# Kernel optimization log

Hardware: AMD Instinct MI355X
Metric: run time of the kernel (lower is better)

The kernel has to match this reference:

```python
import jax, jax.numpy as jnp
import numpy as np

R = 16
ALPHA = 32
SCALING = ALPHA / R  # 2.0


def setup_inputs() -> dict:
    key = jax.random.key(0)
    k_x, k_w, k_b, k_a, k_lb, k_o = jax.random.split(key, 6)
    in_f, out_f = 4096, 4096
    x = jax.random.normal(k_x, (4, 4096, in_f), dtype=jnp.float32)
    base_kernel = jax.random.normal(k_w, (in_f, out_f), dtype=jnp.float32) * 0.02
    base_bias = jax.random.normal(k_b, (out_f,), dtype=jnp.float32) * 0.02
    lora_A = jax.random.normal(k_a, (R, R), dtype=jnp.float32)
    lora_B = jax.random.normal(k_lb, (R, R), dtype=jnp.float32) * 0.02
    O = jax.random.normal(k_o, (in_f // R, out_f // R), dtype=jnp.float32)
    return {"x": x, "base_kernel": base_kernel, "base_bias": base_bias,
            "lora_A": lora_A, "lora_B": lora_B, "O": O}


def reference(x, base_kernel, base_bias, lora_A, lora_B, O) -> jnp.ndarray:
    in_f, out_f = base_kernel.shape
    # base path: x @ W + b
    base_out = jnp.dot(x, base_kernel) + base_bias
    # LoKr path: kron(A @ B, O) materialized as in the original module
    w_left = jnp.dot(lora_A, lora_B)                 # (r, r)
    lokr_update = jnp.kron(w_left, O)                # (r*in_factor, r*out_factor)
    lokr_update = lokr_update[:in_f, :out_f]
    lokr_out = jnp.dot(x, lokr_update)
    return base_out + lokr_out * SCALING
```

## Files before the change

kernel.cpp:

```cpp
#include <hip/hip_runtime.h>
#include <stdint.h>
#include <stddef.h>


#define M_TOT 16384
#define K_TOT 4096
#define N_TOT 4096
#define SCALING 2.0f

typedef __attribute__((ext_vector_type(8))) short bf16x8;
typedef __attribute__((ext_vector_type(4))) float floatx4;

__device__ __forceinline__ unsigned short f32_to_bf16(float f) {
  union { float f; unsigned int u; } v; v.f = f;
  unsigned int r = 0x7fffu + ((v.u >> 16) & 1u);
  return (unsigned short)((v.u + r) >> 16);
}

__device__ __forceinline__ void async_copy16(const void* gsrc, void* ldst) {
  __builtin_amdgcn_global_load_lds(
      (const __attribute__((address_space(1))) void*)(uintptr_t)gsrc,
      (__attribute__((address_space(3))) void*)(uintptr_t)ldst,
      16, 0, 0);
}

__global__ void wleft_kernel(const float* __restrict__ A, const float* __restrict__ B,
                             float* __restrict__ wl) {
  int i = threadIdx.x >> 4, j = threadIdx.x & 15;
  float s = 0.f;
#pragma unroll
  for (int k = 0; k < 16; ++k) s += A[i * 16 + k] * B[k * 16 + j];
  wl[threadIdx.x] = s * SCALING;
}

__global__ void prep_w_kernel(const float* __restrict__ base, const float* __restrict__ O,
                              const float* __restrict__ wl, unsigned short* __restrict__ Wt) {
  __shared__ float tile[32][33];
  int n0 = blockIdx.x * 32, k0 = blockIdx.y * 32;
  int tx = threadIdx.x, ty = threadIdx.y;
#pragma unroll
  for (int r = 0; r < 32; r += 8) {
    int k = k0 + ty + r, n = n0 + tx;
    float v = base[(size_t)k * N_TOT + n]
            + wl[((k >> 8) << 4) + (n >> 8)] * O[((size_t)(k & 255) << 8) + (n & 255)];
    tile[ty + r][tx] = v;
  }
  __syncthreads();
#pragma unroll
  for (int r = 0; r < 32; r += 8) {
    int n = n0 + ty + r, k = k0 + tx;
    Wt[(size_t)n * K_TOT + k] = f32_to_bf16(tile[tx][ty + r]);
  }
}

__global__ void cvt_x_kernel(const float* __restrict__ x, unsigned short* __restrict__ xb) {
  size_t i = ((size_t)blockIdx.x * blockDim.x + threadIdx.x) * 8;
  float4 a = *(const float4*)(x + i);
  float4 b = *(const float4*)(x + i + 4);
  union { bf16x8 v; unsigned short h[8]; } u;
  u.h[0] = f32_to_bf16(a.x); u.h[1] = f32_to_bf16(a.y);
  u.h[2] = f32_to_bf16(a.z); u.h[3] = f32_to_bf16(a.w);
  u.h[4] = f32_to_bf16(b.x); u.h[5] = f32_to_bf16(b.y);
  u.h[6] = f32_to_bf16(b.z); u.h[7] = f32_to_bf16(b.w);
  *(bf16x8*)(xb + i) = u.v;
}

__global__ __launch_bounds__(256) void gemm_bt_kernel(
    const unsigned short* __restrict__ Xb, const unsigned short* __restrict__ Wt,
    const float* __restrict__ bias, float* __restrict__ out) {
  __shared__ __align__(16) unsigned short Alds[128 * 32];
  __shared__ __align__(16) unsigned short Blds[128 * 32];

  const int tid = threadIdx.x;
  const int wave = tid >> 6, lane = tid & 63;
  const int quad = lane >> 4, lanemod = lane & 15;
  const int wm = wave & 1, wn = wave >> 1;

  const int m0 = blockIdx.y * 128, n0 = blockIdx.x * 128;

  floatx4 acc[4][4];
#pragma unroll
  for (int i = 0; i < 4; ++i)
#pragma unroll
    for (int j = 0; j < 4; ++j) acc[i][j] = (floatx4){0.f, 0.f, 0.f, 0.f};

  for (int k0 = 0; k0 < K_TOT; k0 += 32) {
#pragma unroll
    for (int it = 0; it < 2; ++it) {
      int c = it * 256 + tid;
      int row = c >> 2, kc = c & 3;
      async_copy16(Xb + ((size_t)(m0 + row) * K_TOT + k0 + kc * 8), Alds + (size_t)c * 8);
      async_copy16(Wt + ((size_t)(n0 + row) * K_TOT + k0 + kc * 8), Blds + (size_t)c * 8);
    }
    __syncthreads();

    bf16x8 af[4], bfr[4];
#pragma unroll
    for (int t = 0; t < 4; ++t) {
      af[t]  = *(const bf16x8*)(Alds + ((wm * 64 + t * 16 + lanemod) * 32 + quad * 8));
      bfr[t] = *(const bf16x8*)(Blds + ((wn * 64 + t * 16 + lanemod) * 32 + quad * 8));
    }
#pragma unroll
    for (int mt = 0; mt < 4; ++mt)
#pragma unroll
      for (int nt = 0; nt < 4; ++nt)
        acc[mt][nt] = __builtin_amdgcn_mfma_f32_16x16x32_bf16(af[mt], bfr[nt], acc[mt][nt], 0, 0, 0);
    __syncthreads();
  }

#pragma unroll
  for (int nt = 0; nt < 4; ++nt) {
    int col = n0 + wn * 64 + nt * 16 + lanemod;
    float bv = bias[col];
#pragma unroll
    for (int mt = 0; mt < 4; ++mt) {
      int row = m0 + wm * 64 + mt * 16 + quad * 4;
#pragma unroll
      for (int r = 0; r < 4; ++r)
        out[(size_t)(row + r) * N_TOT + col] = acc[mt][nt][r] + bv;
    }
  }
}

extern "C" void kernel_launch(void* const* d_in, const int* in_sizes, int n_in,
                              void* d_out, int out_size, void* d_ws, size_t ws_size,
                              hipStream_t stream) {
  const float* x    = (const float*)d_in[0];
  const float* base = (const float*)d_in[1];
  const float* bias = (const float*)d_in[2];
  const float* lA   = (const float*)d_in[3];
  const float* lB   = (const float*)d_in[4];
  const float* O    = (const float*)d_in[5];
  float* out = (float*)d_out;

  char* ws = (char*)d_ws;
  unsigned short* Xb = (unsigned short*)ws;
  unsigned short* Wt = (unsigned short*)(ws + (size_t)M_TOT * K_TOT * 2);
  float* wl = (float*)(ws + (size_t)M_TOT * K_TOT * 2 + (size_t)N_TOT * K_TOT * 2);

  wleft_kernel<<<1, 256, 0, stream>>>(lA, lB, wl);
  prep_w_kernel<<<dim3(N_TOT / 32, K_TOT / 32), dim3(32, 8), 0, stream>>>(base, O, wl, Wt);
  cvt_x_kernel<<<((size_t)M_TOT * K_TOT) / 8 / 256, 256, 0, stream>>>(x, Xb);
  gemm_bt_kernel<<<dim3(N_TOT / 128, M_TOT / 128), 256, 0, stream>>>(Xb, Wt, bias, out);
}
```

Baseline: 1.121 ms.

## Switch GEMM to 32x32x16 MFMA with swizzled LDS and grouped tile order

The GEMM kernel now uses 32x32x16 bf16 MFMA instructions on 2x2 accumulator tiles instead of 16x16x32 on 4x4 tiles. It XOR-swizzles the LDS layout to avoid bank conflicts on fragment reads, and it precomputes global source pointers that advance by 32 elements per step. Blocks launch on a 1D grid that is remapped so groups of 8 M-tiles share each N tile, which is meant to improve L2 reuse. The aim is to cut LDS read traffic and bank conflicts and raise MFMA throughput. It adds more complex index math and a different output write pattern.

```diff
diff --git a/kernel.cpp b/kernel.cpp
--- a/kernel.cpp
+++ b/kernel.cpp
@@ -9,6 +9,7 @@
 #define SCALING 2.0f
 
 typedef __attribute__((ext_vector_type(8))) short bf16x8;
+typedef __attribute__((ext_vector_type(16))) float floatx16;
 typedef __attribute__((ext_vector_type(4))) float floatx4;
 
 __device__ __forceinline__ unsigned short f32_to_bf16(float f) {
@@ -72,52 +73,75 @@
   __shared__ __align__(16) unsigned short Blds[128 * 32];
 
   const int tid = threadIdx.x;
-  const int wave = tid >> 6, lane = tid & 63;
-  const int quad = lane >> 4, lanemod = lane & 15;
+  const int lane = tid & 63;
+  const int wave = tid >> 6;
+  const int lane31 = lane & 31, khalf = lane >> 5;
   const int wm = wave & 1, wn = wave >> 1;
 
-  const int m0 = blockIdx.y * 128, n0 = blockIdx.x * 128;
+  const int bid = blockIdx.x;
+  const int grp = bid >> 8, loc = bid & 255;
+  const int m0 = (grp * 8 + (loc & 7)) * 128;
+  const int n0 = (loc >> 3) * 128;
 
-  floatx4 acc[4][4];
+  floatx16 acc[2][2];
 #pragma unroll
-  for (int i = 0; i < 4; ++i)
+  for (int i = 0; i < 2; ++i)
 #pragma unroll
-    for (int j = 0; j < 4; ++j) acc[i][j] = (floatx4){0.f, 0.f, 0.f, 0.f};
+    for (int j = 0; j < 2; ++j)
+#pragma unroll
+      for (int r = 0; r < 16; ++r) acc[i][j][r] = 0.f;
+
+  int c0 = tid, c1 = 256 + tid;
+  int r0 = c0 >> 2, s0 = c0 & 3, kc0 = s0 ^ ((r0 >> 1) & 3);
+  int r1 = c1 >> 2, s1 = c1 & 3, kc1 = s1 ^ ((r1 >> 1) & 3);
+  const unsigned short* srcA0 = Xb + (size_t)(m0 + r0) * K_TOT + kc0 * 8;
+  const unsigned short* srcA1 = Xb + (size_t)(m0 + r1) * K_TOT + kc1 * 8;
+  const unsigned short* srcB0 = Wt + (size_t)(n0 + r0) * K_TOT + kc0 * 8;
+  const unsigned short* srcB1 = Wt + (size_t)(n0 + r1) * K_TOT + kc1 * 8;
+
+  int arow0 = wm * 64 + 0 * 32 + lane31, arow1 = wm * 64 + 1 * 32 + lane31;
+  int brow0 = wn * 64 + 0 * 32 + lane31, brow1 = wn * 64 + 1 * 32 + lane31;
+  int aswz0 = (arow0 >> 1) & 3, aswz1 = (arow1 >> 1) & 3;
+  int bswz0 = (brow0 >> 1) & 3, bswz1 = (brow1 >> 1) & 3;
 
   for (int k0 = 0; k0 < K_TOT; k0 += 32) {
-#pragma unroll
-    for (int it = 0; it < 2; ++it) {
-      int c = it * 256 + tid;
-      int row = c >> 2, kc = c & 3;
-      async_copy16(Xb + ((size_t)(m0 + row) * K_TOT + k0 + kc * 8), Alds + (size_t)c * 8);
-      async_copy16(Wt + ((size_t)(n0 + row) * K_TOT + k0 + kc * 8), Blds + (size_t)c * 8);
-    }
+    async_copy16(srcA0, Alds + (size_t)c0 * 8);
+    async_copy16(srcA1, Alds + (size_t)c1 * 8);
+    async_copy16(srcB0, Blds + (size_t)c0 * 8);
+    async_copy16(srcB1, Blds + (size_t)c1 * 8);
+    srcA0 += 32; srcA1 += 32; srcB0 += 32; srcB1 += 32;
     __syncthreads();
 
-    bf16x8 af[4], bfr[4];
 #pragma unroll
-    for (int t = 0; t < 4; ++t) {
-      af[t]  = *(const bf16x8*)(Alds + ((wm * 64 + t * 16 + lanemod) * 32 + quad * 8));
-      bfr[t] = *(const bf16x8*)(Blds + ((wn * 64 + t * 16 + lanemod) * 32 + quad * 8));
+    for (int t = 0; t < 2; ++t) {
+      int jj = 2 * t + khalf;
+      bf16x8 a0 = *(const bf16x8*)(Alds + arow0 * 32 + (jj ^ aswz0) * 8);
+      bf16x8 a1 = *(const bf16x8*)(Alds + arow1 * 32 + (jj ^ aswz1) * 8);
+      bf16x8 b0 = *(const bf16x8*)(Blds + brow0 * 32 + (jj ^ bswz0) * 8);
+      bf16x8 b1 = *(const bf16x8*)(Blds + brow1 * 32 + (jj ^ bswz1) * 8);
+      acc[0][0] = __builtin_amdgcn_mfma_f32_32x32x16_bf16(a0, b0, acc[0][0], 0, 0, 0);
+      acc[0][1] = __builtin_amdgcn_mfma_f32_32x32x16_bf16(a0, b1, acc[0][1], 0, 0, 0);
+      acc[1][0] = __builtin_amdgcn_mfma_f32_32x32x16_bf16(a1, b0, acc[1][0], 0, 0, 0);
+      acc[1][1] = __builtin_amdgcn_mfma_f32_32x32x16_bf16(a1, b1, acc[1][1], 0, 0, 0);
     }
-#pragma unroll
-    for (int mt = 0; mt < 4; ++mt)
-#pragma unroll
-      for (int nt = 0; nt < 4; ++nt)
-        acc[mt][nt] = __builtin_amdgcn_mfma_f32_16x16x32_bf16(af[mt], bfr[nt], acc[mt][nt], 0, 0, 0);
     __syncthreads();
   }
 
 #pragma unroll
-  for (int nt = 0; nt < 4; ++nt) {
-    int col = n0 + wn * 64 + nt * 16 + lanemod;
+  for (int nt = 0; nt < 2; ++nt) {
+    int col = n0 + wn * 64 + nt * 32 + lane31;
     float bv = bias[col];
 #pragma unroll
-    for (int mt = 0; mt < 4; ++mt) {
-      int row = m0 + wm * 64 + mt * 16 + quad * 4;
+    for (int mt = 0; mt < 2; ++mt) {
+      int rowbase = m0 + wm * 64 + mt * 32 + 4 * khalf;
 #pragma unroll
-      for (int r = 0; r < 4; ++r)
-        out[(size_t)(row + r) * N_TOT + col] = acc[mt][nt][r] + bv;
+      for (int rg = 0; rg < 4; ++rg) {
+#pragma unroll
+        for (int rr = 0; rr < 4; ++rr) {
+          int row = rowbase + 8 * rg + rr;
+          out[(size_t)row * N_TOT + col] = acc[mt][nt][rg * 4 + rr] + bv;
+        }
+      }
     }
   }
 }
@@ -141,5 +165,5 @@
   wleft_kernel<<<1, 256, 0, stream>>>(lA, lB, wl);
   prep_w_kernel<<<dim3(N_TOT / 32, K_TOT / 32), dim3(32, 8), 0, stream>>>(base, O, wl, Wt);
   cvt_x_kernel<<<((size_t)M_TOT * K_TOT) / 8 / 256, 256, 0, stream>>>(x, Xb);
-  gemm_bt_kernel<<<dim3(N_TOT / 128, M_TOT / 128), 256, 0, stream>>>(Xb, Wt, bias, out);
+  gemm_bt_kernel<<<(M_TOT / 128) * (N_TOT / 128), 256, 0, stream>>>(Xb, Wt, bias, out);
 }
```

Measured after the change: 1.295 ms. 1.16x slower.

## Double GEMM K-tile to 64 with XOR-swizzled LDS layout and precomputed addresses

Applied to the files above, without the earlier changes.

The GEMM main loop now stages a K-slice of 64 instead of 32 per iteration, so each pair of barriers covers twice as many MFMA instructions. The LDS tile is stored with an XOR swizzle on the 16-byte chunk index to reduce bank conflicts on fragment reads. Global source pointers and LDS offsets are precomputed outside the loop to cut address arithmetic. LDS usage doubles to 32 KB per block, which may reduce occupancy, and loads are still not overlapped with compute.

```diff
diff --git a/kernel.cpp b/kernel.cpp
--- a/kernel.cpp
+++ b/kernel.cpp
@@ -68,8 +68,8 @@
 __global__ __launch_bounds__(256) void gemm_bt_kernel(
     const unsigned short* __restrict__ Xb, const unsigned short* __restrict__ Wt,
     const float* __restrict__ bias, float* __restrict__ out) {
-  __shared__ __align__(16) unsigned short Alds[128 * 32];
-  __shared__ __align__(16) unsigned short Blds[128 * 32];
+  __shared__ __align__(16) unsigned short Alds[128 * 64];
+  __shared__ __align__(16) unsigned short Blds[128 * 64];
 
   const int tid = threadIdx.x;
   const int wave = tid >> 6, lane = tid & 63;
@@ -84,27 +84,51 @@
 #pragma unroll
     for (int j = 0; j < 4; ++j) acc[i][j] = (floatx4){0.f, 0.f, 0.f, 0.f};
 
-  for (int k0 = 0; k0 < K_TOT; k0 += 32) {
+  const unsigned short* srcA[4];
+  const unsigned short* srcB[4];
+  int dst[4];
 #pragma unroll
-    for (int it = 0; it < 2; ++it) {
-      int c = it * 256 + tid;
-      int row = c >> 2, kc = c & 3;
-      async_copy16(Xb + ((size_t)(m0 + row) * K_TOT + k0 + kc * 8), Alds + (size_t)c * 8);
-      async_copy16(Wt + ((size_t)(n0 + row) * K_TOT + k0 + kc * 8), Blds + (size_t)c * 8);
+  for (int it = 0; it < 4; ++it) {
+    int c = it * 256 + tid;
+    int row = c >> 3, kc = (c & 7) ^ (row & 7);
+    srcA[it] = Xb + (size_t)(m0 + row) * K_TOT + kc * 8;
+    srcB[it] = Wt + (size_t)(n0 + row) * K_TOT + kc * 8;
+    dst[it] = c * 8;
+  }
+
+  int aoff[4], bqoff[4], aswz[4], bswz[4];
+#pragma unroll
+  for (int t = 0; t < 4; ++t) {
+    int ar = wm * 64 + t * 16 + lanemod;
+    int br = wn * 64 + t * 16 + lanemod;
+    aoff[t] = ar * 64; aswz[t] = ar & 7;
+    bqoff[t] = br * 64; bswz[t] = br & 7;
+  }
+
+  for (int k0 = 0; k0 < K_TOT; k0 += 64) {
+#pragma unroll
+    for (int it = 0; it < 4; ++it) {
+      async_copy16(srcA[it], Alds + dst[it]);
+      async_copy16(srcB[it], Blds + dst[it]);
+      srcA[it] += 64; srcB[it] += 64;
     }
     __syncthreads();
 
-    bf16x8 af[4], bfr[4];
 #pragma unroll
-    for (int t = 0; t < 4; ++t) {
-      af[t]  = *(const bf16x8*)(Alds + ((wm * 64 + t * 16 + lanemod) * 32 + quad * 8));
-      bfr[t] = *(const bf16x8*)(Blds + ((wn * 64 + t * 16 + lanemod) * 32 + quad * 8));
+    for (int kk = 0; kk < 2; ++kk) {
+      int j = kk * 4 + quad;
+      bf16x8 af[4], bfr[4];
+#pragma unroll
+      for (int t = 0; t < 4; ++t) {
+        af[t]  = *(const bf16x8*)(Alds + aoff[t]  + (j ^ aswz[t]) * 8);
+        bfr[t] = *(const bf16x8*)(Blds + bqoff[t] + (j ^ bswz[t]) * 8);
+      }
+#pragma unroll
+      for (int mt = 0; mt < 4; ++mt)
+#pragma unroll
+        for (int nt = 0; nt < 4; ++nt)
+          acc[mt][nt] = __builtin_amdgcn_mfma_f32_16x16x32_bf16(af[mt], bfr[nt], acc[mt][nt], 0, 0, 0);
     }
-#pragma unroll
-    for (int mt = 0; mt < 4; ++mt)
-#pragma unroll
-      for (int nt = 0; nt < 4; ++nt)
-        acc[mt][nt] = __builtin_amdgcn_mfma_f32_16x16x32_bf16(af[mt], bfr[nt], acc[mt][nt], 0, 0, 0);
     __syncthreads();
   }
 
```

Measured after the change: 1.149 ms. +2.5%, slower.
